# Kernel optimization log

Measured on AMD Instinct MI355X. Metric: run time of the kernel, lower is better.

Reference implementation:

```python
import jax, jax.numpy as jnp
import numpy as np

PAD_TOKEN = 1
V_EN = 32000
V_DE = 32000
WORD_DIM = 300
HID = 500
VLAYER = 500


def lstm(x, Wih, Whh, bih, bhh):
    """Single-layer batch-first LSTM, PyTorch gate order (i,f,g,o). x: [B,T,D] -> h: [B,T,H]."""
    xg = jnp.einsum('btd,gd->btg', x, Wih) + bih  # precompute input projections [B,T,4H]
    H = Whh.shape[1]
    B = x.shape[0]

    def step(carry, xg_t):
        h, c = carry
        g = xg_t + h @ Whh.T + bhh
        i, f, gg, o = jnp.split(g, 4, axis=-1)
        c = jax.nn.sigmoid(f) * c + jax.nn.sigmoid(i) * jnp.tanh(gg)
        h = jax.nn.sigmoid(o) * jnp.tanh(c)
        return (h, c), h

    h0 = jnp.zeros((B, H), x.dtype)
    (_, _), hs = jax.lax.scan(step, (h0, h0), jnp.swapaxes(xg, 0, 1))
    return jnp.swapaxes(hs, 0, 1)


def setup_inputs() -> dict:
    key = jax.random.key(0)
    ks = jax.random.split(key, 12)
    B, S, T = 64, 50, 50
    s = 0.05
    inp = {
        'x_de': jax.random.randint(ks[0], (B, S), 0, V_DE),
        'x_en': jax.random.randint(ks[1], (B, T), 0, V_EN),
        'emb_de_w': jax.random.normal(ks[2], (V_DE, WORD_DIM)) * s,
        'emb_en_w': jax.random.normal(ks[3], (V_EN, WORD_DIM)) * s,
        'enc_Wih': jax.random.normal(ks[4], (4 * HID, WORD_DIM)) * s,
        'enc_Whh': jax.random.normal(ks[5], (4 * HID, HID)) * s,
        'enc_bih': jnp.zeros((4 * HID,)),
        'enc_bhh': jnp.zeros((4 * HID,)),
        'dec_Wih': jax.random.normal(ks[6], (4 * HID, WORD_DIM)) * s,
        'dec_Whh': jax.random.normal(ks[7], (4 * HID, HID)) * s,
        'dec_bih': jnp.zeros((4 * HID,)),
        'dec_bhh': jnp.zeros((4 * HID,)),
        'h2e_w': jax.random.normal(ks[8], (VLAYER, 2 * HID)) * s,
        'h2e_b': jnp.zeros((VLAYER,)),
        'e2v_w': jax.random.normal(ks[9], (V_EN, VLAYER)) * s,
        'e2v_b': jnp.zeros((V_EN,)),
    }
    return inp


def reference(x_de, x_en, emb_de_w, emb_en_w,
              enc_Wih, enc_Whh, enc_bih, enc_bhh,
              dec_Wih, dec_Whh, dec_bih, dec_bhh,
              h2e_w, h2e_b, e2v_w, e2v_b):
    emb_de = emb_de_w[x_de]                       # [B,S,D]
    emb_en = emb_en_w[x_en]                       # [B,T,D]
    enc_h = lstm(emb_de, enc_Wih, enc_Whh, enc_bih, enc_bhh)  # [B,S,H]
    dec_h = lstm(emb_en, dec_Wih, dec_Whh, dec_bih, dec_bhh)  # [B,T,H]

    Tm1 = dec_h.shape[1] - 1
    scores = jnp.einsum('bsh,bth->bst', enc_h, dec_h[:, :Tm1])  # [B,S,T']

    # hard attention: categorical sample per (b,t), all timesteps vectorized
    logp_attn = jax.nn.log_softmax(scores, axis=1)               # [B,S,T']
    samples = jax.random.categorical(jax.random.key(42),
                                     jnp.swapaxes(scores, 1, 2), axis=-1)  # [B,T'] int
    context = jnp.take_along_axis(enc_h, samples[:, :, None], axis=1)      # [B,T',H]

    feat = jnp.concatenate([dec_h[:, :Tm1], context], axis=-1)   # [B,T',2H]
    e = jnp.tanh(feat @ h2e_w.T + h2e_b)
    pred = jax.nn.log_softmax(e @ e2v_w.T + e2v_b, axis=-1)      # [B,T',V]

    y = x_en[:, 1:]                                              # [B,T']
    mask = (y != PAD_TOKEN).astype(pred.dtype)
    reward = jnp.take_along_axis(pred, y[:, :, None], axis=-1)[..., 0]  # [B,T']
    cnt = jnp.maximum(mask.sum(0), 1.0)

    loss = -jnp.sum((reward * mask).sum(0) / cnt)

    logp_s = jnp.take_along_axis(jnp.swapaxes(logp_attn, 1, 2),
                                 samples[:, :, None], axis=-1)[..., 0]  # [B,T']
    baseline = jnp.log(1.0 / V_EN)
    adv = jax.lax.stop_gradient(reward - baseline)
    reinforce_loss = -jnp.sum((logp_s * adv * mask).sum(0) / cnt)

    return loss, reinforce_loss
```

## Files before the change

kernel.cpp:

```cpp
#include <hip/hip_runtime.h>
#include <cstdint>

typedef short short8 __attribute__((ext_vector_type(8)));
typedef float f32x4 __attribute__((ext_vector_type(4)));
typedef uint32_t u32x4 __attribute__((ext_vector_type(4)));
typedef unsigned short u16;
typedef unsigned long long u64;

__device__ __forceinline__ u16 f2bf(float f) {
  union { float f; uint32_t u; } v; v.f = f;
  uint32_t u = v.u;
  uint32_t r = (u + 0x7fffu + ((u >> 16) & 1u)) >> 16;
  return (u16)r;
}
__device__ __forceinline__ float sigm(float x) { return 1.f / (1.f + expf(-x)); }
__device__ __forceinline__ float tanh_f(float x) { return 2.f / (1.f + expf(-2.f * x)) - 1.f; }

typedef const __attribute__((address_space(1))) uint32_t glb_u32;
typedef __attribute__((address_space(3))) uint32_t lds_u32;
__device__ __forceinline__ void glds16(const void* g, void* l) {
  __builtin_amdgcn_global_load_lds((glb_u32*)g, (lds_u32*)l, 16, 0, 0);
}

__device__ __forceinline__ void tfround(uint32_t& a, uint32_t& b, int r) {
  a += b; b = (b << r) | (b >> (32 - r)); b ^= a;
}
__device__ __forceinline__ void threefry(uint32_t k0, uint32_t k1, uint32_t& x0, uint32_t& x1) {
  uint32_t k2 = k0 ^ k1 ^ 0x1BD11BDAu;
  x0 += k0; x1 += k1;
  tfround(x0,x1,13); tfround(x0,x1,15); tfround(x0,x1,26); tfround(x0,x1,6);
  x0 += k1; x1 += k2 + 1u;
  tfround(x0,x1,17); tfround(x0,x1,29); tfround(x0,x1,16); tfround(x0,x1,24);
  x0 += k2; x1 += k0 + 2u;
  tfround(x0,x1,13); tfround(x0,x1,15); tfround(x0,x1,26); tfround(x0,x1,6);
  x0 += k0; x1 += k1 + 3u;
  tfround(x0,x1,17); tfround(x0,x1,29); tfround(x0,x1,16); tfround(x0,x1,24);
  x0 += k1; x1 += k2 + 4u;
  tfround(x0,x1,13); tfround(x0,x1,15); tfround(x0,x1,26); tfround(x0,x1,6);
  x0 += k2; x1 += k0 + 5u;
}
__device__ __forceinline__ float gumbel_from_bits(uint32_t bits) {
  float f = __uint_as_float((bits >> 9) | 0x3f800000u) - 1.0f;
  const float tiny = 1.17549435e-38f;
  float u = fmaxf(f + tiny, tiny);
  return -logf(-logf(u));
}

__global__ __launch_bounds__(256) void prep_all(
    const float* eWih, const float* eWhh, const float* ebih, const float* ebhh,
    const float* dWih, const float* dWhh, const float* dbih, const float* dbhh,
    const float* h2e_w, const float* h2e_b, const float* e2v_w,
    u16* wih_p, u16* whh_p, float* bsum, u16* h2e_p, float* h2e_bp,
    u16* e2v_p, u16* hglob, int* bar)
{
  const uint32_t GWIH = 2u*2048u*40u;
  const uint32_t GWHH = 2u*2048u*64u;
  const uint32_t GBS  = 512u;
  const uint32_t GH2E = 512u*128u;
  const uint32_t GH2EB= 64u;
  const uint32_t GE2V = 32000u*64u;
  const uint32_t GHG  = 16384u;
  const uint32_t GBAR = 64u;
  const uint32_t TOT  = GWIH+GWHH+GBS+GH2E+GH2EB+GE2V+GHG+GBAR;
  for (uint32_t i = blockIdx.x*256u + threadIdx.x; i < TOT; i += gridDim.x*256u) {
    uint32_t j = i;
    if (j < GWIH) {
      uint32_t L = j / (2048u*40u), rem = j % (2048u*40u);
      uint32_t p = rem / 40u, kg = rem % 40u;
      uint32_t g = p >> 9, u = p & 511u, k0 = kg*8u;
      short8 o = {0,0,0,0,0,0,0,0}; u16* op = (u16*)&o;
      if (u < 500u) {
        const float* src = (L ? dWih : eWih) + ((size_t)(g*500u+u))*300u + k0;
        if (k0 + 8u <= 300u) {
          float4 a = *(const float4*)src, b = *(const float4*)(src+4);
          op[0]=f2bf(a.x);op[1]=f2bf(a.y);op[2]=f2bf(a.z);op[3]=f2bf(a.w);
          op[4]=f2bf(b.x);op[5]=f2bf(b.y);op[6]=f2bf(b.z);op[7]=f2bf(b.w);
        } else {
          #pragma unroll
          for (int e = 0; e < 8; ++e) if (k0+e < 300u) op[e] = f2bf(src[e]);
        }
      }
      *(short8*)(wih_p + (size_t)j*8) = o; continue;
    }
    j -= GWIH;
    if (j < GWHH) {
      uint32_t L = j / (2048u*64u), rem = j % (2048u*64u);
      uint32_t row = rem >> 6, kg = rem & 63u, k0 = kg*8u;
      uint32_t wg = row >> 7, r2 = row & 127u, g = r2 >> 5, ul = r2 & 31u;
      uint32_t u = wg*32u + ul;
      short8 o = {0,0,0,0,0,0,0,0}; u16* op = (u16*)&o;
      if (u < 500u) {
        const float* src = (L ? dWhh : eWhh) + ((size_t)(g*500u+u))*500u + k0;
        if (k0 + 8u <= 500u) {
          float4 a = *(const float4*)src, b = *(const float4*)(src+4);
          op[0]=f2bf(a.x);op[1]=f2bf(a.y);op[2]=f2bf(a.z);op[3]=f2bf(a.w);
          op[4]=f2bf(b.x);op[5]=f2bf(b.y);op[6]=f2bf(b.z);op[7]=f2bf(b.w);
        } else {
          #pragma unroll
          for (int e = 0; e < 8; ++e) if (k0+e < 500u) op[e] = f2bf(src[e]);
        }
      }
      *(short8*)(whh_p + (size_t)j*8) = o; continue;
    }
    j -= GWHH;
    if (j < GBS) {
      uint32_t L = j >> 8, pg = j & 255u, p0 = pg*8u;
      float arr[8];
      #pragma unroll
      for (int e = 0; e < 8; ++e) {
        uint32_t p = p0 + e, g = p >> 9, u = p & 511u;
        arr[e] = (u < 500u) ? ((L?dbih:ebih)[g*500u+u] + (L?dbhh:ebhh)[g*500u+u]) : 0.f;
      }
      *(float4*)(bsum + (size_t)j*8) = *(float4*)arr;
      *(float4*)(bsum + (size_t)j*8 + 4) = *(float4*)(arr+4);
      continue;
    }
    j -= GBS;
    if (j < GH2E) {
      uint32_t n = j >> 7, kg = j & 127u, k0 = kg*8u;
      short8 o = {0,0,0,0,0,0,0,0}; u16* op = (u16*)&o;
      if (n < 500u) {
        const float* rowp = h2e_w + (size_t)n*1000u;
        if (k0 + 8u <= 500u) {
          float4 a = *(const float4*)(rowp+k0), b = *(const float4*)(rowp+k0+4);
          op[0]=f2bf(a.x);op[1]=f2bf(a.y);op[2]=f2bf(a.z);op[3]=f2bf(a.w);
          op[4]=f2bf(b.x);op[5]=f2bf(b.y);op[6]=f2bf(b.z);op[7]=f2bf(b.w);
        } else if (k0 >= 512u && k0 + 8u <= 1012u) {
          #pragma unroll
          for (int e = 0; e < 8; ++e) op[e] = f2bf(rowp[k0 + e - 12u]);
        } else {
          #pragma unroll
          for (int e = 0; e < 8; ++e) {
            uint32_t k = k0 + e; float v = 0.f;
            if (k < 500u) v = rowp[k];
            else if (k >= 512u && k < 1012u) v = rowp[k - 12u];
            op[e] = f2bf(v);
          }
        }
      }
      *(short8*)(h2e_p + (size_t)j*8) = o; continue;
    }
    j -= GH2E;
    if (j < GH2EB) {
      uint32_t k0 = j*8u;
      float arr[8];
      #pragma unroll
      for (int e = 0; e < 8; ++e) { uint32_t k = k0+e; arr[e] = (k < 500u) ? h2e_b[k] : 0.f; }
      *(float4*)(h2e_bp + (size_t)j*8) = *(float4*)arr;
      *(float4*)(h2e_bp + (size_t)j*8 + 4) = *(float4*)(arr+4);
      continue;
    }
    j -= GH2EB;
    if (j < GE2V) {
      uint32_t n = j >> 6, kg = j & 63u, k0 = kg*8u;
      short8 o = {0,0,0,0,0,0,0,0}; u16* op = (u16*)&o;
      const float* src = e2v_w + (size_t)n*500u + k0;
      if (k0 + 8u <= 500u) {
        float4 a = *(const float4*)src, b = *(const float4*)(src+4);
        op[0]=f2bf(a.x);op[1]=f2bf(a.y);op[2]=f2bf(a.z);op[3]=f2bf(a.w);
        op[4]=f2bf(b.x);op[5]=f2bf(b.y);op[6]=f2bf(b.z);op[7]=f2bf(b.w);
      } else {
        #pragma unroll
        for (int e = 0; e < 8; ++e) if (k0+e < 500u) op[e] = f2bf(src[e]);
      }
      *(short8*)(e2v_p + (size_t)j*8) = o; continue;
    }
    j -= GE2V;
    if (j < GHG) { short8 z = {0,0,0,0,0,0,0,0}; *(short8*)(hglob + (size_t)j*8) = z; continue; }
    j -= GHG;
    if (j < GBAR) bar[j] = 0;
  }
}

__global__ __launch_bounds__(256, 1) void lstm_kernel(
    const float* xg , const u16* whh_p,
    u16* hglob , float* h_out , int* bar)
{
  const int wg = blockIdx.x;
  const int lstm = wg >> 4;
  const int wgl = wg & 15;
  const int tid = threadIdx.x;
  const int wid = tid >> 6;
  const int lane = tid & 63;

  __shared__ u16 hbuf[64 * 512];
  __shared__ float pre[4][64][34];
  __shared__ u16 hsh[64 * 32];

  short8 wf[2][16];
  {
    const u16* wbase = whh_p + ((size_t)lstm*2048 + wgl*128 + wid*32) * 512;
    #pragma unroll
    for (int nt = 0; nt < 2; ++nt)
      #pragma unroll
      for (int kk = 0; kk < 16; ++kk) {
        int row = nt*16 + (lane & 15);
        int k = kk*32 + (lane >> 4)*8;
        wf[nt][kk] = *(const short8*)(wbase + (size_t)row*512 + k);
      }
  }

  float c[8];
  #pragma unroll
  for (int q = 0; q < 8; ++q) c[q] = 0.f;

  int* mybar = bar + lstm*32;
  const int ug = wgl*32 + (tid & 31);
  const float* xgl = xg + ((size_t)lstm*3200)*2048;

  float xr[4][8];
  #pragma unroll
  for (int q = 0; q < 8; ++q) {
    int b = q*8 + (tid >> 5);
    size_t xrow = ((size_t)(b*50 + 0))*2048;
    #pragma unroll
    for (int g = 0; g < 4; ++g) xr[g][q] = xgl[xrow + g*512 + ug];
  }

  #pragma unroll 1
  for (int t = 0; t < 50; ++t) {
    const int cur = t & 1;
    {
      u32x4 sv[16];
      const char* sbase = (const char*)(hglob + ((size_t)(cur*2 + lstm))*64*512);
      #pragma unroll
      for (int i = 0; i < 16; ++i) {
        const void* p = sbase + (size_t)(i*256 + tid)*16;
        asm volatile("global_load_dwordx4 %0, %1, off sc0 sc1" : "=v"(sv[i]) : "v"(p));
      }
      asm volatile("s_waitcnt vmcnt(0)" ::: "memory");
      __builtin_amdgcn_sched_barrier(0);
      #pragma unroll
      for (int i = 0; i < 16; ++i) {
        int chunk = i*256 + tid;
        int row = chunk >> 5, col16 = chunk & 31;
        int byte = row*1024 + ((col16*16) ^ ((row & 7) << 4));
        *(u32x4*)((char*)hbuf + byte) = sv[i];
      }
    }
    __syncthreads();

    f32x4 zero = {0.f, 0.f, 0.f, 0.f};
    f32x4 acc[4][2];
    #pragma unroll
    for (int m = 0; m < 4; ++m) { acc[m][0] = zero; acc[m][1] = zero; }

    #pragma unroll
    for (int kk = 0; kk < 16; ++kk) {
      short8 af[4];
      #pragma unroll
      for (int m = 0; m < 4; ++m) {
        int row = m*16 + (lane & 15);
        int byte = row*1024 + ((kk*64 + (lane >> 4)*16) ^ ((row & 7) << 4));
        af[m] = *(const short8*)((const char*)hbuf + byte);
      }
      #pragma unroll
      for (int m = 0; m < 4; ++m) {
        acc[m][0] = __builtin_amdgcn_mfma_f32_16x16x32_bf16(af[m], wf[0][kk], acc[m][0], 0, 0, 0);
        acc[m][1] = __builtin_amdgcn_mfma_f32_16x16x32_bf16(af[m], wf[1][kk], acc[m][1], 0, 0, 0);
      }
    }

    #pragma unroll
    for (int m = 0; m < 4; ++m)
      #pragma unroll
      for (int nt = 0; nt < 2; ++nt)
        #pragma unroll
        for (int jj = 0; jj < 4; ++jj) {
          int row = m*16 + (lane >> 4)*4 + jj;
          int col = nt*16 + (lane & 15);
          pre[wid][row][col] = acc[m][nt][jj];
        }
    __syncthreads();

    #pragma unroll
    for (int q = 0; q < 8; ++q) {
      int b = q*8 + (tid >> 5);
      int ul = tid & 31;
      float pi = pre[0][b][ul] + xr[0][q];
      float pf = pre[1][b][ul] + xr[1][q];
      float pg = pre[2][b][ul] + xr[2][q];
      float po = pre[3][b][ul] + xr[3][q];
      c[q] = sigm(pf)*c[q] + sigm(pi)*tanh_f(pg);
      float h = sigm(po)*tanh_f(c[q]);
      if (ug >= 500) h = 0.f;
      h_out[(((size_t)(lstm*64 + b))*50 + t)*512 + ug] = h;
      hsh[b*32 + ul] = f2bf(h);
    }
    if (t == 49) break;
    __syncthreads();

    {
      u16* hdst = hglob + ((size_t)((cur^1)*2 + lstm))*64*512;
      int b2 = tid >> 2, c8 = (tid & 3)*8;
      u32x4 w = *(const u32x4*)(hsh + b2*32 + c8);
      void* dp = hdst + (size_t)b2*512 + wgl*32 + c8;
      asm volatile("global_store_dwordx4 %0, %1, off sc0 sc1" :: "v"(dp), "v"(w) : "memory");
    }
    asm volatile("s_waitcnt vmcnt(0)" ::: "memory");

    if (tid == 0)
      __hip_atomic_fetch_add(mybar, 1, __ATOMIC_RELAXED, __HIP_MEMORY_SCOPE_AGENT);

    {
      const int tn = t + 1;
      #pragma unroll
      for (int q = 0; q < 8; ++q) {
        int b = q*8 + (tid >> 5);
        size_t xrow = ((size_t)(b*50 + tn))*2048;
        #pragma unroll
        for (int g = 0; g < 4; ++g) xr[g][q] = xgl[xrow + g*512 + ug];
      }
    }

    if (tid == 0) {
      int target = 16*(t+1);
      while (__hip_atomic_load(mybar, __ATOMIC_RELAXED, __HIP_MEMORY_SCOPE_AGENT) < target)
        __builtin_amdgcn_s_sleep(1);
    }
    __syncthreads();
  }
}

__global__ __launch_bounds__(256) void scores_kernel(const float* h_out, float* scores) {
  int b = blockIdx.x >> 2, tq = blockIdx.x & 3;
  int tid = threadIdx.x, wid = tid >> 6, lane = tid & 63;
  __shared__ float enc[50*512];
  const float* ebase = h_out + ((size_t)b*50)*512;
  for (int i = tid*4; i < 50*512; i += 256*4)
    *(float4*)(enc + i) = *(const float4*)(ebase + i);
  __syncthreads();
  const int t0 = tq*13;
  const int cnt = (tq == 3) ? 10 : 13;
  for (int tl = wid; tl < cnt; tl += 4) {
    int t = t0 + tl;
    const float* drow = h_out + ((size_t)((64 + b)*50 + t))*512;
    float d[8];
    #pragma unroll
    for (int j = 0; j < 8; ++j) d[j] = drow[lane + j*64];
    for (int s = 0; s < 50; ++s) {
      float p = 0.f;
      #pragma unroll
      for (int j = 0; j < 8; ++j) p += enc[s*512 + lane + j*64] * d[j];
      #pragma unroll
      for (int mk = 32; mk; mk >>= 1) p += __shfl_xor(p, mk);
      if (lane == 0) scores[((size_t)(b*50 + s))*49 + t] = p;
    }
  }
}

__global__ __launch_bounds__(256) void sample_kernel(const float* scores, int* samples, float* logp_s) {
  int p = blockIdx.x*4 + (threadIdx.x >> 6);
  int lane = threadIdx.x & 63;
  int b = p / 49, t = p - b*49;
  float sc = -INFINITY;
  if (lane < 50) sc = scores[((size_t)(b*50 + lane))*49 + t];
  float val = -INFINITY;
  if (lane < 50) {
    uint32_t i = (uint32_t)(p*50 + lane);
    uint32_t x0, x1; int sel;
    if (i < 78400u) { x0 = i; x1 = i + 78400u; sel = 0; }
    else            { x0 = i - 78400u; x1 = i; sel = 1; }
    threefry(0u, 42u, x0, x1);
    val = sc + gumbel_from_bits(sel ? x1 : x0);
  }
  int idx = lane; float v = val;
  #pragma unroll
  for (int mk = 1; mk < 64; mk <<= 1) {
    float ov = __shfl_xor(v, mk);
    int oi = __shfl_xor(idx, mk);
    if (ov > v || (ov == v && oi < idx)) { v = ov; idx = oi; }
  }
  float m = sc;
  #pragma unroll
  for (int mk = 1; mk < 64; mk <<= 1) m = fmaxf(m, __shfl_xor(m, mk));
  float e = (lane < 50) ? expf(sc - m) : 0.f;
  #pragma unroll
  for (int mk = 1; mk < 64; mk <<= 1) e += __shfl_xor(e, mk);
  float lse = m + logf(e);
  float scs = __shfl(sc, idx);
  if (lane == 0) { samples[p] = idx; logp_s[p] = scs - lse; }
}

template <int AMODE, int EPI>
__global__ __launch_bounds__(256) void gemm_k(
    const float* Af32a, const float* Af32b, const int* gia, const int* gib,
    const u16* Abf, const u16* Bp, int ldkB, int KT,
    float* Cf32, u16* Cbf, const float* bias,
    float* pm, float* ps, float* ylogit)
{
  int Mb, Nb;
  if constexpr (EPI == 2) {
    int bid = blockIdx.y*gridDim.x + blockIdx.x;
    const int NBLK = 25*250, q = NBLK/8, r = NBLK%8;
    int xcd = bid & 7, idx = bid >> 3;
    int wgid = (xcd < r ? xcd*(q+1) : r*(q+1) + (xcd-r)*q) + idx;
    Mb = wgid % 25; Nb = wgid / 25;
  } else { Mb = blockIdx.x; Nb = blockIdx.y; }
  const int zb = blockIdx.z;
  const int tid = threadIdx.x;
  const int wid = tid >> 6, lane = tid & 63;
  const int wr = wid >> 1, wc = wid & 1;

  __shared__ u16 As[2*128*64];
  __shared__ u16 Bs[2*128*64];
  __shared__ float part[128][2][2];

  f32x4 zero = {0.f,0.f,0.f,0.f};
  f32x4 acc[4][4];
  #pragma unroll
  for (int m = 0; m < 4; ++m)
    #pragma unroll
    for (int n = 0; n < 4; ++n) acc[m][n] = zero;

  auto MFMA_STEP = [&](int buf) {
    #pragma unroll
    for (int kk2 = 0; kk2 < 2; ++kk2) {
      short8 a[4], b[4];
      #pragma unroll
      for (int m = 0; m < 4; ++m) {
        int row = wr*64 + m*16 + (lane & 15);
        int byte = buf*16384 + row*128 + ((kk2*64 + (lane >> 4)*16) ^ ((row & 7) << 4));
        a[m] = *(const short8*)((const char*)As + byte);
      }
      #pragma unroll
      for (int n = 0; n < 4; ++n) {
        int row = wc*64 + n*16 + (lane & 15);
        int byte = buf*16384 + row*128 + ((kk2*64 + (lane >> 4)*16) ^ ((row & 7) << 4));
        b[n] = *(const short8*)((const char*)Bs + byte);
      }
      #pragma unroll
      for (int m = 0; m < 4; ++m)
        #pragma unroll
        for (int n = 0; n < 4; ++n)
          acc[m][n] = __builtin_amdgcn_mfma_f32_16x16x32_bf16(a[m], b[n], acc[m][n], 0, 0, 0);
    }
  };

  if constexpr (AMODE == 2) {
    auto ISSUE = [&](int it, int buf) {
      #pragma unroll
      for (int i = 0; i < 4; ++i) {
        int chunk = i*256 + tid;
        int row = chunk >> 3, c16 = chunk & 7;
        int cg = c16 ^ (row & 7);
        const u16* sa = Abf + (size_t)(Mb*128 + row)*512 + it*64 + cg*8;
        const u16* sb = Bp  + (size_t)(Nb*128 + row)*512 + it*64 + cg*8;
        char* da = (char*)As + buf*16384 + i*4096 + wid*1024;
        char* db = (char*)Bs + buf*16384 + i*4096 + wid*1024;
        glds16(sa, da);
        glds16(sb, db);
      }
    };
    ISSUE(0, 0);
    asm volatile("s_waitcnt vmcnt(0)" ::: "memory");
    __syncthreads();
    for (int it = 0; it < KT; ++it) {
      const int buf = it & 1;
      if (it + 1 < KT) ISSUE(it + 1, buf ^ 1);
      MFMA_STEP(buf);
      if (it + 1 < KT) {
        asm volatile("s_waitcnt vmcnt(0)" ::: "memory");
        __syncthreads();
      }
    }
  } else {
    const int r = tid >> 1;
    const int koff = (tid & 1)*32;
    const int growA = Mb*128 + r;
    const int growB = Nb*128 + r;

    const float* emb = nullptr; const int* ids = nullptr;
    int fb = 0, ft = 0, fsmp = 0; bool fvalid = true;
    if constexpr (AMODE == 0) {
      emb = zb ? Af32b : Af32a;
      ids = zb ? gib : gia;
    } else {
      fvalid = growA < 3136;
      fb = growA / 49; ft = growA - fb*49;
      fsmp = fvalid ? gia[growA] : 0;
    }

    short8 av8[4], bv8[4];
    auto FETCH = [&](int it) {
      const int k0 = it*64 + koff;
      u16* avp = (u16*)av8;
      if constexpr (AMODE == 0) {
        const float* srow = emb + (size_t)ids[growA]*300;
        #pragma unroll
        for (int j = 0; j < 8; ++j) {
          int k = k0 + j*4;
          float4 v = make_float4(0.f,0.f,0.f,0.f);
          if (k + 4 <= 300) v = *(const float4*)(srow + k);
          avp[j*4+0]=f2bf(v.x); avp[j*4+1]=f2bf(v.y); avp[j*4+2]=f2bf(v.z); avp[j*4+3]=f2bf(v.w);
        }
      } else {
        #pragma unroll
        for (int j = 0; j < 8; ++j) {
          int k = k0 + j*4;
          float4 v = make_float4(0.f,0.f,0.f,0.f);
          if (fvalid) {
            if (k + 4 <= 500) v = *(const float4*)(Af32a + ((size_t)(fb*50 + ft))*512 + k);
            else if (k >= 512 && k + 4 <= 1012) v = *(const float4*)(Af32b + ((size_t)(fb*50 + fsmp))*512 + (k - 512));
          }
          avp[j*4+0]=f2bf(v.x); avp[j*4+1]=f2bf(v.y); avp[j*4+2]=f2bf(v.z); avp[j*4+3]=f2bf(v.w);
        }
      }
      #pragma unroll
      for (int j = 0; j < 4; ++j)
        bv8[j] = *(const short8*)(Bp + (size_t)growB*ldkB + k0 + j*8);
    };
    auto STORE_LDS = [&](int buf) {
      #pragma unroll
      for (int j = 0; j < 4; ++j) {
        int byte = buf*16384 + r*128 + ((koff*2 + j*16) ^ ((r & 7) << 4));
        *(short8*)((char*)As + byte) = av8[j];
        *(short8*)((char*)Bs + byte) = bv8[j];
      }
    };

    FETCH(0);
    STORE_LDS(0);
    __syncthreads();
    for (int it = 0; it < KT; ++it) {
      const int cur = it & 1;
      if (it + 1 < KT) FETCH(it + 1);
      MFMA_STEP(cur);
      __syncthreads();
      if (it + 1 < KT) {
        STORE_LDS(cur ^ 1);
        __syncthreads();
      }
    }
  }

  if constexpr (EPI == 0) {
    float* C = Cf32 + (size_t)zb*3200*2048;
    const float* bs = bias + (size_t)zb*2048;
    #pragma unroll
    for (int m = 0; m < 4; ++m)
      #pragma unroll
      for (int n = 0; n < 4; ++n)
        #pragma unroll
        for (int jj = 0; jj < 4; ++jj) {
          int row = Mb*128 + wr*64 + m*16 + (lane >> 4)*4 + jj;
          int col = Nb*128 + wc*64 + n*16 + (lane & 15);
          C[(size_t)row*2048 + col] = acc[m][n][jj] + bs[col];
        }
  } else if constexpr (EPI == 1) {
    #pragma unroll
    for (int m = 0; m < 4; ++m)
      #pragma unroll
      for (int n = 0; n < 4; ++n)
        #pragma unroll
        for (int jj = 0; jj < 4; ++jj) {
          int row = Mb*128 + wr*64 + m*16 + (lane >> 4)*4 + jj;
          int col = Nb*128 + wc*64 + n*16 + (lane & 15);
          float e = tanh_f(acc[m][n][jj] + bias[col]);
          Cbf[(size_t)row*512 + col] = f2bf(e);
        }
  } else {
    float bias4[4];
    #pragma unroll
    for (int n = 0; n < 4; ++n) bias4[n] = bias[Nb*128 + wc*64 + n*16 + (lane & 15)];
    #pragma unroll
    for (int m = 0; m < 4; ++m)
      #pragma unroll
      for (int jj = 0; jj < 4; ++jj) {
        int trow = wr*64 + m*16 + (lane >> 4)*4 + jj;
        int grow = Mb*128 + trow;
        float x0 = acc[m][0][jj] + bias4[0];
        float x1 = acc[m][1][jj] + bias4[1];
        float x2 = acc[m][2][jj] + bias4[2];
        float x3 = acc[m][3][jj] + bias4[3];
        float mx = fmaxf(fmaxf(x0,x1), fmaxf(x2,x3));
        #pragma unroll
        for (int mk = 1; mk < 16; mk <<= 1) mx = fmaxf(mx, __shfl_xor(mx, mk));
        float sm = expf(x0-mx) + expf(x1-mx) + expf(x2-mx) + expf(x3-mx);
        #pragma unroll
        for (int mk = 1; mk < 16; mk <<= 1) sm += __shfl_xor(sm, mk);
        if (grow < 3136) {
          int b = grow / 49, tt = grow - b*49;
          int yv = gib[b*50 + tt + 1];
          int cb = yv - (Nb*128 + wc*64);
          if (cb == 0*16 + (lane & 15)) ylogit[grow] = x0;
          if (cb == 1*16 + (lane & 15)) ylogit[grow] = x1;
          if (cb == 2*16 + (lane & 15)) ylogit[grow] = x2;
          if (cb == 3*16 + (lane & 15)) ylogit[grow] = x3;
        }
        if ((lane & 15) == 0) { part[trow][wc][0] = mx; part[trow][wc][1] = sm; }
      }
    __syncthreads();
    if (tid < 128) {
      int grow = Mb*128 + tid;
      if (grow < 3136) {
        float m0 = part[tid][0][0], s0 = part[tid][0][1];
        float m1 = part[tid][1][0], s1 = part[tid][1][1];
        float M = fmaxf(m0, m1);
        float S = s0*expf(m0 - M) + s1*expf(m1 - M);
        pm[(size_t)grow*250 + Nb] = M;
        ps[(size_t)grow*250 + Nb] = S;
      }
    }
  }
}

__global__ __launch_bounds__(256) void lse_reduce(const float* pm, const float* ps,
                                                  const float* ylogit, float* reward) {
  int row = blockIdx.x*4 + (threadIdx.x >> 6);
  int lane = threadIdx.x & 63;
  if (row >= 3136) return;
  float M = -INFINITY, S = 0.f;
  for (int j = lane; j < 250; j += 64) {
    float m = pm[(size_t)row*250 + j], s = ps[(size_t)row*250 + j];
    float nm = fmaxf(M, m);
    S = S*expf(M - nm) + s*expf(m - nm);
    M = nm;
  }
  #pragma unroll
  for (int mk = 1; mk < 64; mk <<= 1) {
    float om = __shfl_xor(M, mk), os = __shfl_xor(S, mk);
    float nm = fmaxf(M, om);
    S = S*expf(M - nm) + os*expf(om - nm);
    M = nm;
  }
  if (lane == 0) reward[row] = ylogit[row] - (M + logf(S));
}

__global__ void final_kernel(const float* reward, const float* logp_s, const int* x_en, float* out) {
  int t = threadIdx.x;
  float tl = 0.f, trl = 0.f;
  const float baseline = logf(1.0f / 32000.0f);
  if (t < 49) {
    float sr = 0.f, srl = 0.f; int cm = 0;
    for (int b = 0; b < 64; ++b) {
      int yv = x_en[b*50 + t + 1];
      if (yv != 1) {
        float rw = reward[b*49 + t];
        sr += rw;
        srl += logp_s[b*49 + t] * (rw - baseline);
        cm += 1;
      }
    }
    float cnt = fmaxf((float)cm, 1.f);
    tl = sr / cnt; trl = srl / cnt;
  }
  #pragma unroll
  for (int mk = 1; mk < 64; mk <<= 1) { tl += __shfl_xor(tl, mk); trl += __shfl_xor(trl, mk); }
  if (t == 0) { out[0] = -tl; out[1] = -trl; }
}

extern "C" void kernel_launch(void* const* d_in, const int* in_sizes, int n_in,
                              void* d_out, int out_size, void* d_ws, size_t ws_size,
                              hipStream_t stream) {
  (void)in_sizes; (void)n_in; (void)out_size; (void)ws_size;
  const int*   x_de    = (const int*)d_in[0];
  const int*   x_en    = (const int*)d_in[1];
  const float* emb_de  = (const float*)d_in[2];
  const float* emb_en  = (const float*)d_in[3];
  const float* enc_Wih = (const float*)d_in[4];
  const float* enc_Whh = (const float*)d_in[5];
  const float* enc_bih = (const float*)d_in[6];
  const float* enc_bhh = (const float*)d_in[7];
  const float* dec_Wih = (const float*)d_in[8];
  const float* dec_Whh = (const float*)d_in[9];
  const float* dec_bih = (const float*)d_in[10];
  const float* dec_bhh = (const float*)d_in[11];
  const float* h2e_w   = (const float*)d_in[12];
  const float* h2e_b   = (const float*)d_in[13];
  const float* e2v_w   = (const float*)d_in[14];
  const float* e2v_b   = (const float*)d_in[15];
  float* out = (float*)d_out;

  char* ws = (char*)d_ws;
  size_t o = 0;
  auto alloc = [&](size_t bytes) { size_t rr = o; o += (bytes + 255) & ~(size_t)255; return rr; };
  int*   bar     = (int*)  (ws + alloc(256));
  u16*   wih_p   = (u16*)  (ws + alloc(2ull*2048*320*2));
  u16*   whh_p   = (u16*)  (ws + alloc(2ull*2048*512*2));
  float* bsum    = (float*)(ws + alloc(2ull*2048*4));
  u16*   h2e_p   = (u16*)  (ws + alloc(512ull*1024*2));
  float* h2e_bp  = (float*)(ws + alloc(512ull*4));
  u16*   e2v_p   = (u16*)  (ws + alloc(32000ull*512*2));
  float* xg      = (float*)(ws + alloc(2ull*3200*2048*4));
  u16*   hglob   = (u16*)  (ws + alloc(2ull*2*64*512*2));
  float* h_out   = (float*)(ws + alloc(2ull*64*50*512*4));
  float* scores  = (float*)(ws + alloc(64ull*50*49*4));
  int*   samples = (int*)  (ws + alloc(3136ull*4));
  float* logp_s  = (float*)(ws + alloc(3136ull*4));
  float* ylogit  = (float*)(ws + alloc(3200ull*4));
  float* reward  = (float*)(ws + alloc(3136ull*4));
  u16*   e_buf   = (u16*)  (ws + alloc(3200ull*512*2));
  float* pmb     = (float*)(ws + alloc(3200ull*250*4));
  float* psb     = (float*)(ws + alloc(3200ull*250*4));

  prep_all<<<2048, 256, 0, stream>>>(enc_Wih, enc_Whh, enc_bih, enc_bhh,
      dec_Wih, dec_Whh, dec_bih, dec_bhh, h2e_w, h2e_b, e2v_w,
      wih_p, whh_p, bsum, h2e_p, h2e_bp, e2v_p, hglob, bar);

  gemm_k<0,0><<<dim3(25,16,2), 256, 0, stream>>>(emb_de, emb_en, x_de, x_en,
      nullptr, wih_p, 320, 5, xg, nullptr, bsum, nullptr, nullptr, nullptr);

  lstm_kernel<<<32, 256, 0, stream>>>(xg, whh_p, hglob, h_out, bar);

  scores_kernel<<<256, 256, 0, stream>>>(h_out, scores);

  sample_kernel<<<784, 256, 0, stream>>>(scores, samples, logp_s);

  gemm_k<1,1><<<dim3(25,4,1), 256, 0, stream>>>(h_out + 64ull*50*512, h_out, samples, nullptr,
      nullptr, h2e_p, 1024, 16, nullptr, e_buf, h2e_bp, nullptr, nullptr, nullptr);

  gemm_k<2,2><<<dim3(25,250,1), 256, 0, stream>>>(nullptr, nullptr, nullptr, x_en,
      e_buf, e2v_p, 512, 8, nullptr, nullptr, e2v_b, pmb, psb, ylogit);

  lse_reduce<<<784, 256, 0, stream>>>(pmb, psb, ylogit, reward);

  final_kernel<<<1, 64, 0, stream>>>(reward, logp_s, x_en, out);
}
```

Before: 819.9 us.

## Halve LSTM workgroups to 16 with 512 threads and store input projections in bf16

The recurrent LSTM kernel now runs 8 workgroups per LSTM with 512 threads each instead of 16 with 256. Each workgroup owns 64 hidden units, and the Whh packing layout is remapped to match. This cuts the number of participants in the per-timestep grid barrier and the number of redundant h broadcasts loaded from global memory. Separately, the input-projection GEMM writes xg in bf16 rather than fp32, halving its traffic and the per-step loads in the LSTM. The cost is lower input-projection precision and less total CU parallelism per timestep.

```diff
diff --git a/kernel.cpp b/kernel.cpp
--- a/kernel.cpp
+++ b/kernel.cpp
@@ -12,6 +12,9 @@
   uint32_t u = v.u;
   uint32_t r = (u + 0x7fffu + ((u >> 16) & 1u)) >> 16;
   return (u16)r;
+}
+__device__ __forceinline__ float bf2f(u16 b) {
+  union { uint32_t u; float f; } v; v.u = ((uint32_t)b) << 16; return v.f;
 }
 __device__ __forceinline__ float sigm(float x) { return 1.f / (1.f + expf(-x)); }
 __device__ __forceinline__ float tanh_f(float x) { return 2.f / (1.f + expf(-2.f * x)) - 1.f; }
@@ -86,8 +89,9 @@
     if (j < GWHH) {
       uint32_t L = j / (2048u*64u), rem = j % (2048u*64u);
       uint32_t row = rem >> 6, kg = rem & 63u, k0 = kg*8u;
-      uint32_t wg = row >> 7, r2 = row & 127u, g = r2 >> 5, ul = r2 & 31u;
-      uint32_t u = wg*32u + ul;
+      uint32_t wgl = row >> 8, r2 = row & 255u, w = r2 >> 5, rl = r2 & 31u;
+      uint32_t g = w >> 1;
+      uint32_t u = wgl*64u + (w & 1u)*32u + rl;
       short8 o = {0,0,0,0,0,0,0,0}; u16* op = (u16*)&o;
       if (u < 500u) {
         const float* src = (L ? dWhh : eWhh) + ((size_t)(g*500u+u))*500u + k0;
@@ -172,24 +176,24 @@
   }
 }
 
-__global__ __launch_bounds__(256, 1) void lstm_kernel(
-    const float* xg , const u16* whh_p,
+__global__ __launch_bounds__(512, 1) void lstm_kernel(
+    const u16* xg , const u16* whh_p,
     u16* hglob , float* h_out , int* bar)
 {
   const int wg = blockIdx.x;
-  const int lstm = wg >> 4;
-  const int wgl = wg & 15;
+  const int lstm = wg >> 3;
+  const int wgl = wg & 7;
   const int tid = threadIdx.x;
   const int wid = tid >> 6;
   const int lane = tid & 63;
 
   __shared__ u16 hbuf[64 * 512];
-  __shared__ float pre[4][64][34];
-  __shared__ u16 hsh[64 * 32];
+  __shared__ float pre[4][64][66];
+  __shared__ u16 hsh[64 * 64];
 
   short8 wf[2][16];
   {
-    const u16* wbase = whh_p + ((size_t)lstm*2048 + wgl*128 + wid*32) * 512;
+    const u16* wbase = whh_p + ((size_t)lstm*2048 + wgl*256 + wid*32) * 512;
     #pragma unroll
     for (int nt = 0; nt < 2; ++nt)
       #pragma unroll
@@ -205,35 +209,36 @@
   for (int q = 0; q < 8; ++q) c[q] = 0.f;
 
   int* mybar = bar + lstm*32;
-  const int ug = wgl*32 + (tid & 31);
-  const float* xgl = xg + ((size_t)lstm*3200)*2048;
+  const int ul = tid & 63;
+  const int ug = wgl*64 + ul;
+  const u16* xgl = xg + ((size_t)lstm*3200)*2048;
 
   float xr[4][8];
   #pragma unroll
   for (int q = 0; q < 8; ++q) {
-    int b = q*8 + (tid >> 5);
+    int b = q*8 + (tid >> 6);
     size_t xrow = ((size_t)(b*50 + 0))*2048;
     #pragma unroll
-    for (int g = 0; g < 4; ++g) xr[g][q] = xgl[xrow + g*512 + ug];
+    for (int g = 0; g < 4; ++g) xr[g][q] = bf2f(xgl[xrow + g*512 + ug]);
   }
 
   #pragma unroll 1
   for (int t = 0; t < 50; ++t) {
     const int cur = t & 1;
     {
-      u32x4 sv[16];
+      u32x4 sv[8];
       const char* sbase = (const char*)(hglob + ((size_t)(cur*2 + lstm))*64*512);
       #pragma unroll
-      for (int i = 0; i < 16; ++i) {
-        const void* p = sbase + (size_t)(i*256 + tid)*16;
+      for (int i = 0; i < 8; ++i) {
+        const void* p = sbase + (size_t)(i*512 + tid)*16;
         asm volatile("global_load_dwordx4 %0, %1, off sc0 sc1" : "=v"(sv[i]) : "v"(p));
       }
       asm volatile("s_waitcnt vmcnt(0)" ::: "memory");
       __builtin_amdgcn_sched_barrier(0);
       #pragma unroll
-      for (int i = 0; i < 16; ++i) {
-        int chunk = i*256 + tid;
-        int row = chunk >> 5, col16 = chunk & 31;
+      for (int i = 0; i < 8; ++i) {
+        int chunk = i*512 + tid;
+        int row = chunk >> 6, col16 = chunk & 63;
         int byte = row*1024 + ((col16*16) ^ ((row & 7) << 4));
         *(u32x4*)((char*)hbuf + byte) = sv[i];
       }
@@ -261,22 +266,24 @@
       }
     }
 
-    #pragma unroll
-    for (int m = 0; m < 4; ++m)
-      #pragma unroll
-      for (int nt = 0; nt < 2; ++nt)
-        #pragma unroll
-        for (int jj = 0; jj < 4; ++jj) {
-          int row = m*16 + (lane >> 4)*4 + jj;
-          int col = nt*16 + (lane & 15);
-          pre[wid][row][col] = acc[m][nt][jj];
-        }
+    {
+      const int g = wid >> 1, nh = wid & 1;
+      #pragma unroll
+      for (int m = 0; m < 4; ++m)
+        #pragma unroll
+        for (int nt = 0; nt < 2; ++nt)
+          #pragma unroll
+          for (int jj = 0; jj < 4; ++jj) {
+            int row = m*16 + (lane >> 4)*4 + jj;
+            int col = nh*32 + nt*16 + (lane & 15);
+            pre[g][row][col] = acc[m][nt][jj];
+          }
+    }
     __syncthreads();
 
     #pragma unroll
     for (int q = 0; q < 8; ++q) {
-      int b = q*8 + (tid >> 5);
-      int ul = tid & 31;
+      int b = q*8 + (tid >> 6);
       float pi = pre[0][b][ul] + xr[0][q];
       float pf = pre[1][b][ul] + xr[1][q];
       float pg = pre[2][b][ul] + xr[2][q];
@@ -285,16 +292,16 @@
       float h = sigm(po)*tanh_f(c[q]);
       if (ug >= 500) h = 0.f;
       h_out[(((size_t)(lstm*64 + b))*50 + t)*512 + ug] = h;
-      hsh[b*32 + ul] = f2bf(h);
+      hsh[b*64 + ul] = f2bf(h);
     }
     if (t == 49) break;
     __syncthreads();
 
     {
       u16* hdst = hglob + ((size_t)((cur^1)*2 + lstm))*64*512;
-      int b2 = tid >> 2, c8 = (tid & 3)*8;
-      u32x4 w = *(const u32x4*)(hsh + b2*32 + c8);
-      void* dp = hdst + (size_t)b2*512 + wgl*32 + c8;
+      int b2 = tid >> 3, c8 = (tid & 7)*8;
+      u32x4 w = *(const u32x4*)(hsh + tid*8);
+      void* dp = hdst + (size_t)b2*512 + wgl*64 + c8;
       asm volatile("global_store_dwordx4 %0, %1, off sc0 sc1" :: "v"(dp), "v"(w) : "memory");
     }
     asm volatile("s_waitcnt vmcnt(0)" ::: "memory");
@@ -306,15 +313,15 @@
       const int tn = t + 1;
       #pragma unroll
       for (int q = 0; q < 8; ++q) {
-        int b = q*8 + (tid >> 5);
+        int b = q*8 + (tid >> 6);
         size_t xrow = ((size_t)(b*50 + tn))*2048;
         #pragma unroll
-        for (int g = 0; g < 4; ++g) xr[g][q] = xgl[xrow + g*512 + ug];
+        for (int g = 0; g < 4; ++g) xr[g][q] = bf2f(xgl[xrow + g*512 + ug]);
       }
     }
 
     if (tid == 0) {
-      int target = 16*(t+1);
+      int target = 8*(t+1);
       while (__hip_atomic_load(mybar, __ATOMIC_RELAXED, __HIP_MEMORY_SCOPE_AGENT) < target)
         __builtin_amdgcn_s_sleep(1);
     }
@@ -535,7 +542,7 @@
   }
 
   if constexpr (EPI == 0) {
-    float* C = Cf32 + (size_t)zb*3200*2048;
+    u16* C = Cbf + (size_t)zb*3200*2048;
     const float* bs = bias + (size_t)zb*2048;
     #pragma unroll
     for (int m = 0; m < 4; ++m)
@@ -545,7 +552,7 @@
         for (int jj = 0; jj < 4; ++jj) {
           int row = Mb*128 + wr*64 + m*16 + (lane >> 4)*4 + jj;
           int col = Nb*128 + wc*64 + n*16 + (lane & 15);
-          C[(size_t)row*2048 + col] = acc[m][n][jj] + bs[col];
+          C[(size_t)row*2048 + col] = f2bf(acc[m][n][jj] + bs[col]);
         }
   } else if constexpr (EPI == 1) {
     #pragma unroll
@@ -682,7 +689,7 @@
   u16*   h2e_p   = (u16*)  (ws + alloc(512ull*1024*2));
   float* h2e_bp  = (float*)(ws + alloc(512ull*4));
   u16*   e2v_p   = (u16*)  (ws + alloc(32000ull*512*2));
-  float* xg      = (float*)(ws + alloc(2ull*3200*2048*4));
+  u16*   xg      = (u16*)  (ws + alloc(2ull*3200*2048*2));
   u16*   hglob   = (u16*)  (ws + alloc(2ull*2*64*512*2));
   float* h_out   = (float*)(ws + alloc(2ull*64*50*512*4));
   float* scores  = (float*)(ws + alloc(64ull*50*49*4));
@@ -699,9 +706,9 @@
       wih_p, whh_p, bsum, h2e_p, h2e_bp, e2v_p, hglob, bar);
 
   gemm_k<0,0><<<dim3(25,16,2), 256, 0, stream>>>(emb_de, emb_en, x_de, x_en,
-      nullptr, wih_p, 320, 5, xg, nullptr, bsum, nullptr, nullptr, nullptr);
-
-  lstm_kernel<<<32, 256, 0, stream>>>(xg, whh_p, hglob, h_out, bar);
+      nullptr, wih_p, 320, 5, nullptr, xg, bsum, nullptr, nullptr, nullptr);
+
+  lstm_kernel<<<16, 512, 0, stream>>>(xg, whh_p, hglob, h_out, bar);
 
   scores_kernel<<<256, 256, 0, stream>>>(h_out, scores);
 
```

After: 935.8 us. +14.1%, slower.
